# Kernel optimization log

Measured on AMD Instinct MI355X. Metric: run time of the kernel, lower is better.

Reference implementation:

```python
import jax, jax.numpy as jnp
import numpy as np
from jax import lax

B, S, W = 64, 64, 12          # batch, sentences, words-per-sentence (max_seq)
V, SYM, HID = 32000, 128, 256  # vocab, symbol_size, hidden_size
E, R = 64, 32                  # entity_size, role_size
EPS = 1e-5


def _mlp(x, W1, b1, W2, b2):
    # equation 'b...e,er->b...r' is a matmul on the last axis; tanh hidden, linear out
    return jnp.tanh(x @ W1 + b1) @ W2 + b2


def _ln(x, g, b):
    mu = jnp.mean(x, axis=-1, keepdims=True)
    var = jnp.mean(jnp.square(x - mu), axis=-1, keepdims=True)
    return (x - mu) * lax.rsqrt(var + EPS) * g + b


def setup_inputs() -> dict:
    key = jax.random.key(0)
    ks = jax.random.split(key, 24)
    s_in = 1.0 / np.sqrt(SYM)
    s_h = 1.0 / np.sqrt(HID)
    inp = {
        "story": jax.random.randint(ks[0], (B, S, W), 0, V),
        "query": jax.random.randint(ks[1], (B, W), 0, V),
        "word_embed": jax.random.uniform(ks[2], (V, SYM), jnp.float32, -0.1, 0.1),
        "pos_embed": jnp.ones((W, SYM), jnp.float32) / W,
        # UpdateModule MLPs: 2 entity heads (out=E), 3 role heads (out=R), stacked
        "ue_W1": jax.random.normal(ks[3], (2, SYM, HID)) * s_in,
        "ue_b1": jnp.zeros((2, HID), jnp.float32),
        "ue_W2": jax.random.normal(ks[4], (2, HID, E)) * s_h,
        "ue_b2": jnp.zeros((2, E), jnp.float32),
        "ur_W1": jax.random.normal(ks[5], (3, SYM, HID)) * s_in,
        "ur_b1": jnp.zeros((3, HID), jnp.float32),
        "ur_W2": jax.random.normal(ks[6], (3, HID, R)) * s_h,
        "ur_b2": jnp.zeros((3, R), jnp.float32),
        # InferenceModule MLPs
        "ie_W1": jax.random.normal(ks[7], (2, SYM, HID)) * s_in,
        "ie_b1": jnp.zeros((2, HID), jnp.float32),
        "ie_W2": jax.random.normal(ks[8], (2, HID, E)) * s_h,
        "ie_b2": jnp.zeros((2, E), jnp.float32),
        "ir_W1": jax.random.normal(ks[9], (3, SYM, HID)) * s_in,
        "ir_b1": jnp.zeros((3, HID), jnp.float32),
        "ir_W2": jax.random.normal(ks[10], (3, HID, R)) * s_h,
        "ir_b2": jnp.zeros((3, R), jnp.float32),
        "ln_g": jnp.ones((3, E), jnp.float32),
        "ln_b": jnp.zeros((3, E), jnp.float32),
        "Z": jax.random.normal(ks[11], (E, V)) * (1.0 / np.sqrt(E)),
    }
    return inp


def reference(story, query, word_embed, pos_embed,
              ue_W1, ue_b1, ue_W2, ue_b2, ur_W1, ur_b1, ur_W2, ur_b2,
              ie_W1, ie_b1, ie_W2, ie_b2, ir_W1, ir_b1, ir_W2, ir_b2,
              ln_g, ln_b, Z):
    # ---- InputModule ----
    sent = jnp.einsum('bswe,we->bse', word_embed[story], pos_embed)   # [B,S,SYM]
    qsum = jnp.einsum('bwe,we->be', word_embed[query], pos_embed)     # [B,SYM]

    # ---- UpdateModule: precompute per-step entity/role vectors ----
    e1 = _mlp(sent, ue_W1[0], ue_b1[0], ue_W2[0], ue_b2[0])  # [B,S,E]
    e2 = _mlp(sent, ue_W1[1], ue_b1[1], ue_W2[1], ue_b2[1])
    r1 = _mlp(sent, ur_W1[0], ur_b1[0], ur_W2[0], ur_b2[0])  # [B,S,R]
    r2 = _mlp(sent, ur_W1[1], ur_b1[1], ur_W2[1], ur_b2[1])
    r3 = _mlp(sent, ur_W1[2], ur_b1[2], ur_W2[2], ur_b2[2])
    paW = jnp.einsum('bsr,bsf->bsrf', r1, e2)
    paB = jnp.einsum('bsr,bsf->bsrf', r3, e1)

    xs = tuple(jnp.moveaxis(t, 1, 0) for t in (e1, r1, paW, e2, r2, paB, r3))

    def step(TPR, x):
        e1i, r1i, paWi, e2i, r2i, paBi, r3i = x
        t1 = jnp.einsum('be,berf->brf', e1i, TPR)
        w_hat = jnp.einsum('br,brf->bf', r1i, t1)
        m_hat = jnp.einsum('br,brf->bf', r2i, t1)
        b_hat = jnp.einsum('be,br,berf->bf', e2i, r3i, TPR)
        write_op = paWi - r1i[:, :, None] * w_hat[:, None, :]
        move_op = r2i[:, :, None] * (w_hat - m_hat)[:, None, :]
        back_op = paBi - r3i[:, :, None] * b_hat[:, None, :]
        delta = (jnp.einsum('be,brf->berf', e1i, write_op + move_op)
                 + jnp.einsum('be,brf->berf', e2i, back_op))
        return TPR + delta, None

    TPR0 = jnp.zeros((sent.shape[0], E, R, E), sent.dtype)
    TPR, _ = lax.scan(step, TPR0, xs)

    # ---- InferenceModule ----
    qe1 = _mlp(qsum, ie_W1[0], ie_b1[0], ie_W2[0], ie_b2[0])
    qr1 = _mlp(qsum, ir_W1[0], ir_b1[0], ir_W2[0], ir_b2[0])
    qr2 = _mlp(qsum, ir_W1[1], ir_b1[1], ir_W2[1], ir_b2[1])
    qr3 = _mlp(qsum, ir_W1[2], ir_b1[2], ir_W2[2], ir_b2[2])
    i1 = _ln(jnp.einsum('be,br,berf->bf', qe1, qr1, TPR), ln_g[0], ln_b[0])
    i2 = _ln(jnp.einsum('be,br,berf->bf', i1, qr2, TPR), ln_g[1], ln_b[1])
    i3 = _ln(jnp.einsum('be,br,berf->bf', i2, qr3, TPR), ln_g[2], ln_b[2])
    return (i1 + i2 + i3) @ Z
```

## Files before the change

### kernel.cpp

```cpp
#include <hip/hip_runtime.h>
#include <math.h>

#define B_   64
#define S_   64
#define W_   12
#define V_   32000
#define SYM_ 128
#define HID_ 256
#define E_   64
#define R_   32

typedef short bf16x8 __attribute__((ext_vector_type(8)));
typedef float f32x4 __attribute__((ext_vector_type(4)));
#define MFMA16 __builtin_amdgcn_mfma_f32_16x16x32_bf16

__device__ __forceinline__ float fast_tanh(float x) {
  float e = __expf(2.0f * x);
  return 1.0f - 2.0f * __builtin_amdgcn_rcpf(e + 1.0f);
}

__device__ __forceinline__ void split1(float x, unsigned short& h, unsigned short& l) {
  unsigned u = __float_as_uint(x);
  h = (unsigned short)(u >> 16);
  float r = x - __uint_as_float(u & 0xFFFF0000u);
  unsigned v = __float_as_uint(r);
  l = (unsigned short)((v + 0x7FFFu + ((v >> 16) & 1u)) >> 16);
}

__device__ __forceinline__ void split8(const float4& a, const float4& b,
                                       bf16x8& h8, bf16x8& l8) {
  float xs[8] = {a.x, a.y, a.z, a.w, b.x, b.y, b.z, b.w};
#pragma unroll
  for (int j = 0; j < 8; ++j) {
    unsigned short hh, ll;
    split1(xs[j], hh, ll);
    h8[j] = (short)hh;
    l8[j] = (short)ll;
  }
}

__global__ __launch_bounds__(128) void k_embed(
    const int* __restrict__ story, const int* __restrict__ query,
    const float* __restrict__ we, const float* __restrict__ pe,
    float* __restrict__ X) {
  int row = blockIdx.x;
  int e = threadIdx.x;
  const int* idx = (row < 4096) ? story + row * W_ : query + (row - 4096) * W_;
  float acc = 0.f;
#pragma unroll
  for (int w = 0; w < W_; ++w)
    acc = fmaf(we[(long)idx[w] * SYM_ + e], pe[w * SYM_ + e], acc);
  X[row * SYM_ + e] = acc;
}

__global__ __launch_bounds__(64) void k_wprep(
    const float* __restrict__ ueW1, const float* __restrict__ urW1,
    const float* __restrict__ ieW1, const float* __restrict__ irW1,
    const float* __restrict__ ueW2, const float* __restrict__ urW2,
    const float* __restrict__ ieW2, const float* __restrict__ irW2,
    unsigned short* __restrict__ w1ph, unsigned short* __restrict__ w1pl,
    unsigned short* __restrict__ w2ph, unsigned short* __restrict__ w2pl) {
  int l = threadIdx.x;
  int bid = blockIdx.x;
  bf16x8 h8, l8;
  if (bid < 640) {
    int slot = bid >> 6, rem = bid & 63;
    int nt = rem >> 2, ks = rem & 3;
    int grp = slot / 5, h = slot % 5;
    const float* src = (h < 2) ? ((grp ? ieW1 : ueW1) + h * (SYM_ * HID_))
                               : ((grp ? irW1 : urW1) + (h - 2) * (SYM_ * HID_));
    int kk = ks * 32 + (l >> 4) * 8;
    int n = nt * 16 + (l & 15);
#pragma unroll
    for (int j = 0; j < 8; ++j) {
      unsigned short hh, ll;
      split1(src[(long)(kk + j) * HID_ + n], hh, ll);
      h8[j] = (short)hh;
      l8[j] = (short)ll;
    }
    long dst = ((long)(slot * 16 + nt) * 4 + ks) * 512 + l * 8;
    *(bf16x8*)(w1ph + dst) = h8;
    *(bf16x8*)(w1pl + dst) = l8;
  } else {
    int fid = bid - 640;
    int slot = fid >> 5, rem = fid & 31;
    int nt = rem >> 3, ks = rem & 7;
    int grp = slot / 5, h = slot % 5;
    bool isE = h < 2;
    if (!isE && nt >= 2) return;
    int NC = isE ? E_ : R_;
    const float* src = isE ? ((grp ? ieW2 : ueW2) + h * (HID_ * E_))
                           : ((grp ? irW2 : urW2) + (h - 2) * (HID_ * R_));
    int kk = ks * 32 + (l >> 4) * 8;
    int n = nt * 16 + (l & 15);
#pragma unroll
    for (int j = 0; j < 8; ++j) {
      unsigned short hh, ll;
      split1(src[(long)(kk + j) * NC + n], hh, ll);
      h8[j] = (short)hh;
      l8[j] = (short)ll;
    }
    long dst = ((long)(slot * 4 + nt) * 8 + ks) * 512 + l * 8;
    *(bf16x8*)(w2ph + dst) = h8;
    *(bf16x8*)(w2pl + dst) = l8;
  }
}

__global__ __launch_bounds__(256) void k_mlp(
    const float* __restrict__ X,
    const unsigned short* __restrict__ w1ph, const unsigned short* __restrict__ w1pl,
    const unsigned short* __restrict__ w2ph, const unsigned short* __restrict__ w2pl,
    const float* __restrict__ ueb1, const float* __restrict__ urb1,
    const float* __restrict__ ieb1, const float* __restrict__ irb1,
    const float* __restrict__ ueb2, const float* __restrict__ urb2,
    const float* __restrict__ ieb2, const float* __restrict__ irb2,
    float* __restrict__ oE0, float* __restrict__ oE1,
    float* __restrict__ oR0, float* __restrict__ oR1, float* __restrict__ oR2) {
  __shared__ unsigned short Hhi[32][264];
  __shared__ unsigned short Hlo[32][264];

  int h = blockIdx.x % 5;
  int tile = blockIdx.x / 5;
  int rowbase = tile * 32;
  int grp = (rowbase >= 4096) ? 1 : 0;
  bool isE = (h < 2);
  int slot = grp * 5 + h;
  const float* b1 = isE ? ((grp ? ieb1 : ueb1) + h * HID_)
                        : ((grp ? irb1 : urb1) + (h - 2) * HID_);
  const float* b2 = isE ? ((grp ? ieb2 : ueb2) + h * E_)
                        : ((grp ? irb2 : urb2) + (h - 2) * R_);
  float* out = (h == 0) ? oE0 : (h == 1) ? oE1 : (h == 2) ? oR0 : (h == 3) ? oR1 : oR2;

  int tid = threadIdx.x;
  int w = tid >> 6;
  int l = tid & 63;
  int lr = l & 15;
  int lk = l >> 4;

  f32x4 acc[2][4];
#pragma unroll
  for (int mt = 0; mt < 2; ++mt)
#pragma unroll
    for (int ntl = 0; ntl < 4; ++ntl) acc[mt][ntl] = (f32x4){0.f, 0.f, 0.f, 0.f};

  const unsigned short* w1hS = w1ph + (long)slot * 32768 + l * 8;
  const unsigned short* w1lS = w1pl + (long)slot * 32768 + l * 8;

#pragma unroll
  for (int ks = 0; ks < 4; ++ks) {
    bf16x8 ah[2], al[2];
#pragma unroll
    for (int mt = 0; mt < 2; ++mt) {
      const float* xp = X + (long)(rowbase + mt * 16 + lr) * SYM_ + ks * 32 + lk * 8;
      float4 x0 = *(const float4*)xp;
      float4 x1 = *(const float4*)(xp + 4);
      split8(x0, x1, ah[mt], al[mt]);
    }
#pragma unroll
    for (int ntl = 0; ntl < 4; ++ntl) {
      int nt = 4 * w + ntl;
      long fo = ((long)nt * 4 + ks) * 512;
      bf16x8 bh = *(const bf16x8*)(w1hS + fo);
      bf16x8 bl = *(const bf16x8*)(w1lS + fo);
#pragma unroll
      for (int mt = 0; mt < 2; ++mt) {
        acc[mt][ntl] = MFMA16(ah[mt], bh, acc[mt][ntl], 0, 0, 0);
        acc[mt][ntl] = MFMA16(ah[mt], bl, acc[mt][ntl], 0, 0, 0);
        acc[mt][ntl] = MFMA16(al[mt], bh, acc[mt][ntl], 0, 0, 0);
      }
    }
  }

#pragma unroll
  for (int ntl = 0; ntl < 4; ++ntl) {
    int col = (4 * w + ntl) * 16 + lr;
    float bb = b1[col];
#pragma unroll
    for (int mt = 0; mt < 2; ++mt)
#pragma unroll
      for (int reg = 0; reg < 4; ++reg) {
        float t = fast_tanh(acc[mt][ntl][reg] + bb);
        unsigned short hh, ll;
        split1(t, hh, ll);
        int row = mt * 16 + lk * 4 + reg;
        Hhi[row][col] = hh;
        Hlo[row][col] = ll;
      }
  }
  __syncthreads();

  if (isE) {
    const unsigned short* w2hS = w2ph + (long)slot * 16384 + l * 8;
    const unsigned short* w2lS = w2pl + (long)slot * 16384 + l * 8;
    int nt2 = w;
    f32x4 acc2[2];
    acc2[0] = (f32x4){0.f, 0.f, 0.f, 0.f};
    acc2[1] = (f32x4){0.f, 0.f, 0.f, 0.f};
#pragma unroll
    for (int ks2 = 0; ks2 < 8; ++ks2) {
      long fo = ((long)nt2 * 8 + ks2) * 512;
      bf16x8 bh = *(const bf16x8*)(w2hS + fo);
      bf16x8 bl = *(const bf16x8*)(w2lS + fo);
#pragma unroll
      for (int mt = 0; mt < 2; ++mt) {
        int row = mt * 16 + lr, kh = ks2 * 32 + lk * 8;
        bf16x8 ah2 = *(const bf16x8*)&Hhi[row][kh];
        bf16x8 al2 = *(const bf16x8*)&Hlo[row][kh];
        acc2[mt] = MFMA16(ah2, bh, acc2[mt], 0, 0, 0);
        acc2[mt] = MFMA16(ah2, bl, acc2[mt], 0, 0, 0);
        acc2[mt] = MFMA16(al2, bh, acc2[mt], 0, 0, 0);
      }
    }
    int col2 = nt2 * 16 + lr;
    float bb2 = b2[col2];
#pragma unroll
    for (int mt = 0; mt < 2; ++mt)
#pragma unroll
      for (int reg = 0; reg < 4; ++reg)
        out[(long)(rowbase + mt * 16 + lk * 4 + reg) * E_ + col2] = acc2[mt][reg] + bb2;
  } else {
    const unsigned short* w2hS = w2ph + (long)slot * 16384 + l * 8;
    const unsigned short* w2lS = w2pl + (long)slot * 16384 + l * 8;
    int mt = w >> 1, nt2 = w & 1;
    f32x4 acc2 = (f32x4){0.f, 0.f, 0.f, 0.f};
#pragma unroll
    for (int ks2 = 0; ks2 < 8; ++ks2) {
      long fo = ((long)nt2 * 8 + ks2) * 512;
      bf16x8 bh = *(const bf16x8*)(w2hS + fo);
      bf16x8 bl = *(const bf16x8*)(w2lS + fo);
      int row = mt * 16 + lr, kh = ks2 * 32 + lk * 8;
      bf16x8 ah2 = *(const bf16x8*)&Hhi[row][kh];
      bf16x8 al2 = *(const bf16x8*)&Hlo[row][kh];
      acc2 = MFMA16(ah2, bh, acc2, 0, 0, 0);
      acc2 = MFMA16(ah2, bl, acc2, 0, 0, 0);
      acc2 = MFMA16(al2, bh, acc2, 0, 0, 0);
    }
    int col2 = nt2 * 16 + lr;
    float bb2 = b2[col2];
#pragma unroll
    for (int reg = 0; reg < 4; ++reg)
      out[(long)(rowbase + mt * 16 + lk * 4 + reg) * R_ + col2] = acc2[reg] + bb2;
  }
}

__global__ __launch_bounds__(256) void k_gram(
    const float* __restrict__ e1, const float* __restrict__ e2,
    const float* __restrict__ r1, const float* __restrict__ r2,
    const float* __restrict__ r3, float* __restrict__ Wt) {
  int b = blockIdx.x / 9, m = blockIdx.x % 9;
  const float* sE = ((m < 6) ? e1 : e2) + (long)b * S_ * E_;
  const float* jE = ((m == 2 || m == 5 || m == 8) ? e2 : e1) + (long)b * S_ * E_;
  int sk = m / 3, jk = m % 3;
  const float* sR = ((sk == 0) ? r1 : (sk == 1) ? r2 : r3) + (long)b * S_ * R_;
  const float* jR = ((jk == 0) ? r1 : (jk == 1) ? r2 : r3) + (long)b * S_ * R_;

  __shared__ float Es[64][68], Ej[64][68], Rs[64][36], Rj[64][36];
  int tid = threadIdx.x;
  for (int i = tid; i < 1024; i += 256) {
    int row = i >> 4, c = i & 15;
    *(float4*)&Es[row][4 * c] = *(const float4*)(sE + row * 64 + 4 * c);
    *(float4*)&Ej[row][4 * c] = *(const float4*)(jE + row * 64 + 4 * c);
  }
  for (int i = tid; i < 512; i += 256) {
    int row = i >> 3, c = i & 7;
    *(float4*)&Rs[row][4 * c] = *(const float4*)(sR + row * 32 + 4 * c);
    *(float4*)&Rj[row][4 * c] = *(const float4*)(jR + row * 32 + 4 * c);
  }
  __syncthreads();

  int s0 = (tid & 15) * 4, j0 = (tid >> 4) * 4;
  float ed[4][4] = {}, rd[4][4] = {};
#pragma unroll 4
  for (int k = 0; k < 16; ++k) {
    float4 es[4], ej[4];
#pragma unroll
    for (int i = 0; i < 4; ++i) {
      es[i] = *(const float4*)&Es[s0 + i][4 * k];
      ej[i] = *(const float4*)&Ej[j0 + i][4 * k];
    }
#pragma unroll
    for (int i = 0; i < 4; ++i)
#pragma unroll
      for (int j = 0; j < 4; ++j)
        ed[i][j] = fmaf(es[i].x, ej[j].x, fmaf(es[i].y, ej[j].y,
                   fmaf(es[i].z, ej[j].z, fmaf(es[i].w, ej[j].w, ed[i][j]))));
  }
#pragma unroll 4
  for (int k = 0; k < 8; ++k) {
    float4 rs[4], rj[4];
#pragma unroll
    for (int i = 0; i < 4; ++i) {
      rs[i] = *(const float4*)&Rs[s0 + i][4 * k];
      rj[i] = *(const float4*)&Rj[j0 + i][4 * k];
    }
#pragma unroll
    for (int i = 0; i < 4; ++i)
#pragma unroll
      for (int j = 0; j < 4; ++j)
        rd[i][j] = fmaf(rs[i].x, rj[j].x, fmaf(rs[i].y, rj[j].y,
                   fmaf(rs[i].z, rj[j].z, fmaf(rs[i].w, rj[j].w, rd[i][j]))));
  }
  float* wout = Wt + (long)(b * 9 + m) * 4096;
#pragma unroll
  for (int jj = 0; jj < 4; ++jj) {
    float4 o4 = make_float4(ed[0][jj] * rd[0][jj], ed[1][jj] * rd[1][jj],
                            ed[2][jj] * rd[2][jj], ed[3][jj] * rd[3][jj]);
    *(float4*)(wout + (j0 + jj) * 64 + s0) = o4;
  }
}

__global__ __launch_bounds__(256) void k_scan(
    const float* __restrict__ e1g, const float* __restrict__ e2g,
    const float* __restrict__ Wt, float4* __restrict__ acd) {
  __shared__ float WtL[9 * 512];
  int b = blockIdx.x & 63;
  int g = blockIdx.x >> 6;
  int tid = threadIdx.x;
  int wv = tid >> 6;
  int lane = tid & 63;
  int f0 = g * 8 + wv * 2;
  int f1 = f0 + 1;
  const float* Wb = Wt + (long)b * 9 * 4096;
  long eoff = ((long)b * 64 + lane) * 64;
  float e1x = e1g[eoff + f0], e1y = e1g[eoff + f1];
  float e2x = e2g[eoff + f0], e2y = e2g[eoff + f1];

  float pW0 = 0.f, pM0 = 0.f, pB0 = 0.f;
  float pW1 = 0.f, pM1 = 0.f, pB1 = 0.f;
  float ca0 = e2x, cc0 = 0.f, cd0 = e1x;
  float ca1 = e2y, cc1 = 0.f, cd1 = e1y;
  float ka0 = 0.f, kc0 = 0.f, kd0 = 0.f;
  float ka1 = 0.f, kc1 = 0.f, kd1 = 0.f;

  for (int jc = 0; jc < 8; ++jc) {
    __syncthreads();
    for (int i = tid; i < 1152; i += 256) {
      int m = i >> 7;
      int off = (i & 127) * 4;
      *(float4*)&WtL[m * 512 + off] = *(const float4*)(Wb + m * 4096 + jc * 512 + off);
    }
    __syncthreads();
#pragma unroll
    for (int jj = 0; jj < 8; ++jj) {
      int j = jc * 8 + jj;
      float wa = WtL[0 * 512 + jj * 64 + lane];
      float wc = WtL[1 * 512 + jj * 64 + lane];
      float wd = WtL[2 * 512 + jj * 64 + lane];
      float ma = WtL[3 * 512 + jj * 64 + lane];
      float mc = WtL[4 * 512 + jj * 64 + lane];
      float md = WtL[5 * 512 + jj * 64 + lane];
      float ba = WtL[6 * 512 + jj * 64 + lane];
      float bc = WtL[7 * 512 + jj * 64 + lane];
      float bd = WtL[8 * 512 + jj * 64 + lane];
      float aj0 = __int_as_float(__builtin_amdgcn_readlane(__float_as_int(ca0), j));
      float cj0 = __int_as_float(__builtin_amdgcn_readlane(__float_as_int(cc0), j));
      float dj0 = __int_as_float(__builtin_amdgcn_readlane(__float_as_int(cd0), j));
      float aj1 = __int_as_float(__builtin_amdgcn_readlane(__float_as_int(ca1), j));
      float cj1 = __int_as_float(__builtin_amdgcn_readlane(__float_as_int(cc1), j));
      float dj1 = __int_as_float(__builtin_amdgcn_readlane(__float_as_int(cd1), j));
      bool own = (lane == j);
      ka0 = own ? ca0 : ka0; kc0 = own ? cc0 : kc0; kd0 = own ? cd0 : kd0;
      ka1 = own ? ca1 : ka1; kc1 = own ? cc1 : kc1; kd1 = own ? cd1 : kd1;
      pW0 = fmaf(wa, aj0, pW0); pW0 = fmaf(wc, cj0, pW0); pW0 = fmaf(wd, dj0, pW0);
      pM0 = fmaf(ma, aj0, pM0); pM0 = fmaf(mc, cj0, pM0); pM0 = fmaf(md, dj0, pM0);
      pB0 = fmaf(ba, aj0, pB0); pB0 = fmaf(bc, cj0, pB0); pB0 = fmaf(bd, dj0, pB0);
      pW1 = fmaf(wa, aj1, pW1); pW1 = fmaf(wc, cj1, pW1); pW1 = fmaf(wd, dj1, pW1);
      pM1 = fmaf(ma, aj1, pM1); pM1 = fmaf(mc, cj1, pM1); pM1 = fmaf(md, dj1, pM1);
      pB1 = fmaf(ba, aj1, pB1); pB1 = fmaf(bc, cj1, pB1); pB1 = fmaf(bd, dj1, pB1);
      ca0 = e2x - pW0; cc0 = pW0 - pM0; cd0 = e1x - pB0;
      ca1 = e2y - pW1; cc1 = pW1 - pM1; cd1 = e1y - pB1;
    }
  }
  acd[eoff + f0] = make_float4(ka0, kc0, kd0, 0.f);
  acd[eoff + f1] = make_float4(ka1, kc1, kd1, 0.f);
}

__global__ __launch_bounds__(1024) void k_infer(
    const float4* __restrict__ acd,
    const float* __restrict__ e1, const float* __restrict__ e2,
    const float* __restrict__ r1, const float* __restrict__ r2,
    const float* __restrict__ r3,
    const float* __restrict__ qe1, const float* __restrict__ qr1,
    const float* __restrict__ qr2, const float* __restrict__ qr3,
    const float* __restrict__ lng, const float* __restrict__ lnb,
    float* __restrict__ isum) {
  int b = blockIdx.x, tid = threadIdx.x;
  __shared__ float hista[64 * 65], histc[64 * 65], histd[64 * 65];
  __shared__ float vlds[9 * 64];
  __shared__ float ivec[64];
  __shared__ float u1s[64], u2s[64];
  __shared__ float dsc[64];

  {
    const float4* ab = acd + (long)b * 4096;
    for (int idx = tid; idx < 4096; idx += 1024) {
      float4 hv = ab[idx];
      int j = idx >> 6, f = idx & 63;
      hista[j * 65 + f] = hv.x;
      histc[j * 65 + f] = hv.y;
      histd[j * 65 + f] = hv.z;
    }
  }
  if (tid < 576) {
    int pk = tid >> 6, j = tid & 63;
    int p = pk / 3, k = pk % 3;
    const float* rv = ((k == 0) ? r1 : (k == 1) ? r2 : r3) + ((long)b * 64 + j) * 32;
    const float* q = ((p == 0) ? qr1 : (p == 1) ? qr2 : qr3) + b * 32;
    float acc = 0.f;
#pragma unroll
    for (int t = 0; t < 8; ++t) {
      float4 rv4 = *(const float4*)(rv + 4 * t);
      float4 q4 = *(const float4*)(q + 4 * t);
      acc = fmaf(rv4.x, q4.x, fmaf(rv4.y, q4.y,
            fmaf(rv4.z, q4.z, fmaf(rv4.w, q4.w, acc))));
    }
    vlds[pk * 64 + j] = acc;
  }
  if (tid < 64) ivec[tid] = qe1[b * 64 + tid];
  __syncthreads();

  int f = tid >> 4, jsl = tid & 15;
  int dotd = tid >> 3, dt = tid & 7;
  int which = dotd >> 6, dj = dotd & 63;
  const float* erow = (which ? e2 : e1) + ((long)b * 64 + dj) * 64 + dt * 8;
  float isacc = 0.f;
  for (int p = 0; p < 3; ++p) {
    {
      float acc = 0.f;
#pragma unroll
      for (int t = 0; t < 8; ++t)
        acc = fmaf(erow[t], ivec[dt * 8 + t], acc);
      acc += __shfl_xor(acc, 1, 64);
      acc += __shfl_xor(acc, 2, 64);
      acc += __shfl_xor(acc, 4, 64);
      if (dt == 0) { if (which) u2s[dj] = acc; else u1s[dj] = acc; }
    }
    __syncthreads();
    float part = 0.f;
#pragma unroll
    for (int i = 0; i < 4; ++i) {
      int j = jsl * 4 + i;
      float ca = u1s[j] * vlds[(p * 3 + 0) * 64 + j];
      float cc = u1s[j] * vlds[(p * 3 + 1) * 64 + j];
      float cd = u2s[j] * vlds[(p * 3 + 2) * 64 + j];
      part = fmaf(ca, hista[j * 65 + f],
             fmaf(cc, histc[j * 65 + f],
             fmaf(cd, histd[j * 65 + f], part)));
    }
    part += __shfl_xor(part, 1, 64);
    part += __shfl_xor(part, 2, 64);
    part += __shfl_xor(part, 4, 64);
    part += __shfl_xor(part, 8, 64);
    if (jsl == 0) dsc[f] = part;
    __syncthreads();
    if (tid < 64) {
      float v = dsc[tid];
      float mu = v;
#pragma unroll
      for (int mm = 1; mm <= 32; mm <<= 1) mu += __shfl_xor(mu, mm, 64);
      mu *= (1.f / 64.f);
      float d = v - mu;
      float vr = d * d;
#pragma unroll
      for (int mm = 1; mm <= 32; mm <<= 1) vr += __shfl_xor(vr, mm, 64);
      vr *= (1.f / 64.f);
      float iv = d * (1.f / sqrtf(vr + 1e-5f)) * lng[p * 64 + tid] + lnb[p * 64 + tid];
      ivec[tid] = iv;
      isacc += iv;
    }
    __syncthreads();
  }
  if (tid < 64) isum[b * 64 + tid] = isacc;
}

__global__ __launch_bounds__(256) void k_final(
    const float* __restrict__ isum, const float* __restrict__ Zm,
    float* __restrict__ out) {
  __shared__ float isT[64 * 68];
  int tid = threadIdx.x;
  for (int i = tid; i < 4096; i += 256) {
    int bb = i >> 6, e = i & 63;
    isT[e * 68 + bb] = isum[i];
  }
  __syncthreads();
  int tr = tid >> 4, tc = tid & 15;
  int v0 = blockIdx.x * 64 + tc * 4;
  float acc[4][4] = {};
#pragma unroll 2
  for (int e = 0; e < 64; ++e) {
    float4 a4 = *(const float4*)&isT[e * 68 + 4 * tr];
    float4 z4 = *(const float4*)(Zm + (long)e * V_ + v0);
    float as[4] = {a4.x, a4.y, a4.z, a4.w};
    float zs[4] = {z4.x, z4.y, z4.z, z4.w};
#pragma unroll
    for (int i = 0; i < 4; ++i)
#pragma unroll
      for (int j = 0; j < 4; ++j) acc[i][j] = fmaf(as[i], zs[j], acc[i][j]);
  }
#pragma unroll
  for (int i = 0; i < 4; ++i) {
    float4 o4 = make_float4(acc[i][0], acc[i][1], acc[i][2], acc[i][3]);
    *(float4*)(out + (long)(4 * tr + i) * V_ + v0) = o4;
  }
}

extern "C" void kernel_launch(void* const* d_in, const int* in_sizes, int n_in,
                              void* d_out, int out_size, void* d_ws, size_t ws_size,
                              hipStream_t stream) {
  const int* story = (const int*)d_in[0];
  const int* query = (const int*)d_in[1];
  const float* we = (const float*)d_in[2];
  const float* pe = (const float*)d_in[3];
  const float* ueW1 = (const float*)d_in[4];
  const float* ueb1 = (const float*)d_in[5];
  const float* ueW2 = (const float*)d_in[6];
  const float* ueb2 = (const float*)d_in[7];
  const float* urW1 = (const float*)d_in[8];
  const float* urb1 = (const float*)d_in[9];
  const float* urW2 = (const float*)d_in[10];
  const float* urb2 = (const float*)d_in[11];
  const float* ieW1 = (const float*)d_in[12];
  const float* ieb1 = (const float*)d_in[13];
  const float* ieW2 = (const float*)d_in[14];
  const float* ieb2 = (const float*)d_in[15];
  const float* irW1 = (const float*)d_in[16];
  const float* irb1 = (const float*)d_in[17];
  const float* irW2 = (const float*)d_in[18];
  const float* irb2 = (const float*)d_in[19];
  const float* lng = (const float*)d_in[20];
  const float* lnb = (const float*)d_in[21];
  const float* Zm = (const float*)d_in[22];

  float* ws = (float*)d_ws;
  float* X = ws;
  float* e1 = X + 532480;
  float* e2 = e1 + 266240;
  float* r1 = e2 + 266240;
  float* r2 = r1 + 133120;
  float* r3 = r2 + 133120;
  float* isum = r3 + 133120;
  float* Wt = isum + 4096;
  float4* acd = (float4*)(Wt + 2359296);
  float* qe1 = e1 + 4096 * 64;
  float* qr1 = r1 + 4096 * 32;
  float* qr2 = r2 + 4096 * 32;
  float* qr3 = r3 + 4096 * 32;
  float* outF = (float*)d_out;

  unsigned short* w1ph = (unsigned short*)Wt;
  unsigned short* w1pl = w1ph + 327680;
  unsigned short* w2ph = w1pl + 327680;
  unsigned short* w2pl = w2ph + 163840;

  k_embed<<<4160, 128, 0, stream>>>(story, query, we, pe, X);
  k_wprep<<<960, 64, 0, stream>>>(ueW1, urW1, ieW1, irW1, ueW2, urW2, ieW2, irW2,
                                  w1ph, w1pl, w2ph, w2pl);
  k_mlp<<<130 * 5, 256, 0, stream>>>(X, w1ph, w1pl, w2ph, w2pl,
                                     ueb1, urb1, ieb1, irb1,
                                     ueb2, urb2, ieb2, irb2,
                                     e1, e2, r1, r2, r3);
  k_gram<<<64 * 9, 256, 0, stream>>>(e1, e2, r1, r2, r3, Wt);
  k_scan<<<512, 256, 0, stream>>>(e1, e2, Wt, acd);
  k_infer<<<B_, 1024, 0, stream>>>(acd, e1, e2, r1, r2, r3, qe1, qr1, qr2, qr3,
                                   lng, lnb, isum);
  k_final<<<V_ / 64, 256, 0, stream>>>(isum, Zm, outF);
}
```

Before: 197.9 us.

## Fuse embed and weight-prep kernels; widen scan to four columns per lane

The embedding and weight-preparation kernels are merged into one launch, which removes one kernel launch and its gap. The scan kernel now handles four f-columns per lane instead of two and runs on half as many blocks. Its LDS tile is transposed to [jj][lane][9], so each lane reads its nine coefficients with vector loads rather than nine scalar LDS reads. More work now shares each LDS load and broadcast, at the cost of higher register pressure and fewer blocks to fill the GPU.

```diff
diff --git a/kernel.cpp b/kernel.cpp
--- a/kernel.cpp
+++ b/kernel.cpp
@@ -19,6 +19,10 @@
   return 1.0f - 2.0f * __builtin_amdgcn_rcpf(e + 1.0f);
 }
 
+__device__ __forceinline__ float bcastf(float v, int lane) {
+  return __int_as_float(__builtin_amdgcn_readlane(__float_as_int(v), lane));
+}
+
 __device__ __forceinline__ void split1(float x, unsigned short& h, unsigned short& l) {
   unsigned u = __float_as_uint(x);
   h = (unsigned short)(u >> 16);
@@ -39,29 +43,30 @@
   }
 }
 
-__global__ __launch_bounds__(128) void k_embed(
+__global__ __launch_bounds__(128) void k_prep(
     const int* __restrict__ story, const int* __restrict__ query,
     const float* __restrict__ we, const float* __restrict__ pe,
-    float* __restrict__ X) {
-  int row = blockIdx.x;
-  int e = threadIdx.x;
-  const int* idx = (row < 4096) ? story + row * W_ : query + (row - 4096) * W_;
-  float acc = 0.f;
-#pragma unroll
-  for (int w = 0; w < W_; ++w)
-    acc = fmaf(we[(long)idx[w] * SYM_ + e], pe[w * SYM_ + e], acc);
-  X[row * SYM_ + e] = acc;
-}
-
-__global__ __launch_bounds__(64) void k_wprep(
+    float* __restrict__ X,
     const float* __restrict__ ueW1, const float* __restrict__ urW1,
     const float* __restrict__ ieW1, const float* __restrict__ irW1,
     const float* __restrict__ ueW2, const float* __restrict__ urW2,
     const float* __restrict__ ieW2, const float* __restrict__ irW2,
     unsigned short* __restrict__ w1ph, unsigned short* __restrict__ w1pl,
     unsigned short* __restrict__ w2ph, unsigned short* __restrict__ w2pl) {
+  if (blockIdx.x < 4160) {
+    int row = blockIdx.x;
+    int e = threadIdx.x;
+    const int* idx = (row < 4096) ? story + row * W_ : query + (row - 4096) * W_;
+    float acc = 0.f;
+#pragma unroll
+    for (int w = 0; w < W_; ++w)
+      acc = fmaf(we[(long)idx[w] * SYM_ + e], pe[w * SYM_ + e], acc);
+    X[row * SYM_ + e] = acc;
+    return;
+  }
   int l = threadIdx.x;
-  int bid = blockIdx.x;
+  if (l >= 64) return;
+  int bid = blockIdx.x - 4160;
   bf16x8 h8, l8;
   if (bid < 640) {
     int slot = bid >> 6, rem = bid & 63;
@@ -312,67 +317,72 @@
 __global__ __launch_bounds__(256) void k_scan(
     const float* __restrict__ e1g, const float* __restrict__ e2g,
     const float* __restrict__ Wt, float4* __restrict__ acd) {
-  __shared__ float WtL[9 * 512];
+  __shared__ float WtL[8][64][12];
   int b = blockIdx.x & 63;
-  int g = blockIdx.x >> 6;
+  int gq = blockIdx.x >> 6;
   int tid = threadIdx.x;
   int wv = tid >> 6;
   int lane = tid & 63;
-  int f0 = g * 8 + wv * 2;
-  int f1 = f0 + 1;
+  int fbase = gq * 16 + wv * 4;
   const float* Wb = Wt + (long)b * 9 * 4096;
   long eoff = ((long)b * 64 + lane) * 64;
-  float e1x = e1g[eoff + f0], e1y = e1g[eoff + f1];
-  float e2x = e2g[eoff + f0], e2y = e2g[eoff + f1];
-
-  float pW0 = 0.f, pM0 = 0.f, pB0 = 0.f;
-  float pW1 = 0.f, pM1 = 0.f, pB1 = 0.f;
-  float ca0 = e2x, cc0 = 0.f, cd0 = e1x;
-  float ca1 = e2y, cc1 = 0.f, cd1 = e1y;
-  float ka0 = 0.f, kc0 = 0.f, kd0 = 0.f;
-  float ka1 = 0.f, kc1 = 0.f, kd1 = 0.f;
+  float4 e1v = *(const float4*)(e1g + eoff + fbase);
+  float4 e2v = *(const float4*)(e2g + eoff + fbase);
+  float e1a[4] = {e1v.x, e1v.y, e1v.z, e1v.w};
+  float e2a[4] = {e2v.x, e2v.y, e2v.z, e2v.w};
+
+  float pW[4], pM[4], pB[4], ca[4], cc[4], cd[4], ka[4], kc[4], kd[4];
+#pragma unroll
+  for (int f = 0; f < 4; ++f) {
+    pW[f] = pM[f] = pB[f] = 0.f;
+    ka[f] = kc[f] = kd[f] = 0.f;
+    ca[f] = e2a[f]; cc[f] = 0.f; cd[f] = e1a[f];
+  }
 
   for (int jc = 0; jc < 8; ++jc) {
     __syncthreads();
-    for (int i = tid; i < 1152; i += 256) {
-      int m = i >> 7;
-      int off = (i & 127) * 4;
-      *(float4*)&WtL[m * 512 + off] = *(const float4*)(Wb + m * 4096 + jc * 512 + off);
+#pragma unroll
+    for (int t = 0; t < 2; ++t) {
+      int jj = wv * 2 + t;
+      const float* src = Wb + jc * 512 + jj * 64 + lane;
+      float v[9];
+#pragma unroll
+      for (int m = 0; m < 9; ++m) v[m] = src[m * 4096];
+      float* dst = &WtL[jj][lane][0];
+      *(float4*)dst = make_float4(v[0], v[1], v[2], v[3]);
+      *(float4*)(dst + 4) = make_float4(v[4], v[5], v[6], v[7]);
+      dst[8] = v[8];
     }
     __syncthreads();
 #pragma unroll
     for (int jj = 0; jj < 8; ++jj) {
       int j = jc * 8 + jj;
-      float wa = WtL[0 * 512 + jj * 64 + lane];
-      float wc = WtL[1 * 512 + jj * 64 + lane];
-      float wd = WtL[2 * 512 + jj * 64 + lane];
-      float ma = WtL[3 * 512 + jj * 64 + lane];
-      float mc = WtL[4 * 512 + jj * 64 + lane];
-      float md = WtL[5 * 512 + jj * 64 + lane];
-      float ba = WtL[6 * 512 + jj * 64 + lane];
-      float bc = WtL[7 * 512 + jj * 64 + lane];
-      float bd = WtL[8 * 512 + jj * 64 + lane];
-      float aj0 = __int_as_float(__builtin_amdgcn_readlane(__float_as_int(ca0), j));
-      float cj0 = __int_as_float(__builtin_amdgcn_readlane(__float_as_int(cc0), j));
-      float dj0 = __int_as_float(__builtin_amdgcn_readlane(__float_as_int(cd0), j));
-      float aj1 = __int_as_float(__builtin_amdgcn_readlane(__float_as_int(ca1), j));
-      float cj1 = __int_as_float(__builtin_amdgcn_readlane(__float_as_int(cc1), j));
-      float dj1 = __int_as_float(__builtin_amdgcn_readlane(__float_as_int(cd1), j));
+      const float* wrow = &WtL[jj][lane][0];
+      float4 w03 = *(const float4*)wrow;
+      float4 w47 = *(const float4*)(wrow + 4);
+      float bd = wrow[8];
+      float wa = w03.x, wc = w03.y, wd = w03.z;
+      float ma = w03.w, mc = w47.x, md = w47.y;
+      float ba = w47.z, bc = w47.w;
       bool own = (lane == j);
-      ka0 = own ? ca0 : ka0; kc0 = own ? cc0 : kc0; kd0 = own ? cd0 : kd0;
-      ka1 = own ? ca1 : ka1; kc1 = own ? cc1 : kc1; kd1 = own ? cd1 : kd1;
-      pW0 = fmaf(wa, aj0, pW0); pW0 = fmaf(wc, cj0, pW0); pW0 = fmaf(wd, dj0, pW0);
-      pM0 = fmaf(ma, aj0, pM0); pM0 = fmaf(mc, cj0, pM0); pM0 = fmaf(md, dj0, pM0);
-      pB0 = fmaf(ba, aj0, pB0); pB0 = fmaf(bc, cj0, pB0); pB0 = fmaf(bd, dj0, pB0);
-      pW1 = fmaf(wa, aj1, pW1); pW1 = fmaf(wc, cj1, pW1); pW1 = fmaf(wd, dj1, pW1);
-      pM1 = fmaf(ma, aj1, pM1); pM1 = fmaf(mc, cj1, pM1); pM1 = fmaf(md, dj1, pM1);
-      pB1 = fmaf(ba, aj1, pB1); pB1 = fmaf(bc, cj1, pB1); pB1 = fmaf(bd, dj1, pB1);
-      ca0 = e2x - pW0; cc0 = pW0 - pM0; cd0 = e1x - pB0;
-      ca1 = e2y - pW1; cc1 = pW1 - pM1; cd1 = e1y - pB1;
-    }
-  }
-  acd[eoff + f0] = make_float4(ka0, kc0, kd0, 0.f);
-  acd[eoff + f1] = make_float4(ka1, kc1, kd1, 0.f);
+#pragma unroll
+      for (int f = 0; f < 4; ++f) {
+        float aj = bcastf(ca[f], j);
+        float cj = bcastf(cc[f], j);
+        float dj = bcastf(cd[f], j);
+        ka[f] = own ? ca[f] : ka[f];
+        kc[f] = own ? cc[f] : kc[f];
+        kd[f] = own ? cd[f] : kd[f];
+        pW[f] = fmaf(wa, aj, pW[f]); pW[f] = fmaf(wc, cj, pW[f]); pW[f] = fmaf(wd, dj, pW[f]);
+        pM[f] = fmaf(ma, aj, pM[f]); pM[f] = fmaf(mc, cj, pM[f]); pM[f] = fmaf(md, dj, pM[f]);
+        pB[f] = fmaf(ba, aj, pB[f]); pB[f] = fmaf(bc, cj, pB[f]); pB[f] = fmaf(bd, dj, pB[f]);
+        ca[f] = e2a[f] - pW[f]; cc[f] = pW[f] - pM[f]; cd[f] = e1a[f] - pB[f];
+      }
+    }
+  }
+#pragma unroll
+  for (int f = 0; f < 4; ++f)
+    acd[eoff + fbase + f] = make_float4(ka[f], kc[f], kd[f], 0.f);
 }
 
 __global__ __launch_bounds__(1024) void k_infer(
@@ -552,15 +562,16 @@
   unsigned short* w2ph = w1pl + 327680;
   unsigned short* w2pl = w2ph + 163840;
 
-  k_embed<<<4160, 128, 0, stream>>>(story, query, we, pe, X);
-  k_wprep<<<960, 64, 0, stream>>>(ueW1, urW1, ieW1, irW1, ueW2, urW2, ieW2, irW2,
-                                  w1ph, w1pl, w2ph, w2pl);
+  k_prep<<<4160 + 960, 128, 0, stream>>>(story, query, we, pe, X,
+                                         ueW1, urW1, ieW1, irW1,
+                                         ueW2, urW2, ieW2, irW2,
+                                         w1ph, w1pl, w2ph, w2pl);
   k_mlp<<<130 * 5, 256, 0, stream>>>(X, w1ph, w1pl, w2ph, w2pl,
                                      ueb1, urb1, ieb1, irb1,
                                      ueb2, urb2, ieb2, irb2,
                                      e1, e2, r1, r2, r3);
   k_gram<<<64 * 9, 256, 0, stream>>>(e1, e2, r1, r2, r3, Wt);
-  k_scan<<<512, 256, 0, stream>>>(e1, e2, Wt, acd);
+  k_scan<<<256, 256, 0, stream>>>(e1, e2, Wt, acd);
   k_infer<<<B_, 1024, 0, stream>>>(acd, e1, e2, r1, r2, r3, qe1, qr1, qr2, qr3,
                                    lng, lnb, isum);
   k_final<<<V_ / 64, 256, 0, stream>>>(isum, Zm, outF);
```

After: 194.6 us. No clear change (-1.6%).
